# Kernel tuning notes

Hardware: AMD Instinct MI355X
Metric: run time of the kernel (lower is better)

The kernel has to match this reference:

```python
import jax, jax.numpy as jnp
import numpy as np

B, SE, SD, IN_DIM, D, DEPTH, H, DH, M, FF, NBINS = 8, 2048, 1024, 1280, 512, 4, 8, 64, 266, 2048, 128

def _ln(x, g, b):
    mu = x.mean(-1, keepdims=True)
    var = ((x - mu) ** 2).mean(-1, keepdims=True)
    return (x - mu) / jnp.sqrt(var + 1e-5) * g + b

def _gelu(x):
    return jax.nn.gelu(x, approximate=False)

def _sinusoidal(x, dim):
    # sinusoidal embedding of integer expression bins -> [.., dim]
    half = dim // 2
    freqs = jnp.exp(-jnp.log(10000.0) * jnp.arange(half, dtype=jnp.float32) / half)
    ang = x[..., None].astype(jnp.float32) * freqs
    return jnp.concatenate([jnp.sin(ang), jnp.cos(ang)], axis=-1)

def _split_heads(x):
    b, s, _ = x.shape
    return x.reshape(b, s, H, DH).transpose(0, 2, 1, 3)

def _merge_heads(x):
    b, h, s, d = x.shape
    return x.transpose(0, 2, 1, 3).reshape(b, s, h * d)

def _favor_attention(q, k, v, proj):
    # FAVOR+ softmax-kernel linear attention (non-causal), performer-style
    dn = DH ** -0.25
    ratio = M ** -0.5
    eps = 1e-4
    qd = jnp.einsum('bhsd,md->bhsm', q * dn, proj)
    kd = jnp.einsum('bhsd,md->bhsm', k * dn, proj)
    q_diag = 0.5 * (q ** 2).sum(-1, keepdims=True) * dn * dn
    k_diag = 0.5 * (k ** 2).sum(-1, keepdims=True) * dn * dn
    qp = ratio * (jnp.exp(qd - q_diag - jnp.max(qd, axis=-1, keepdims=True)) + eps)
    kp = ratio * (jnp.exp(kd - k_diag - jnp.max(kd)) + eps)
    k_sum = kp.sum(axis=2)                                   # [b,h,m]
    d_inv = 1.0 / jnp.einsum('bhsm,bhm->bhs', qp, k_sum)     # [b,h,s]
    kv = jnp.einsum('bhsm,bhsd->bhmd', kp, v)                # [b,h,m,d]
    return jnp.einsum('bhsm,bhmd->bhsd', qp, kv) * d_inv[..., None]

def _forward(var_input_encoder, var_input_decoder, var_W, var_b, enc_ln_g, enc_ln_b, dec_ln_g, dec_ln_b, p_ln1_g, p_ln1_b, p_Wq, p_Wk, p_Wv, p_Wo, p_bo, p_ln2_g, p_ln2_b, p_w1, p_b1, p_w2, p_b2, proj, ca_Wq, ca_Wk, ca_Wv, ca_Wo, ca_bo, cross_ln_g, cross_ln_b, ffd_w1, ffd_b1, ffd_w2, ffd_b2, out_ln_g, out_ln_b, head_W, head_b, expression_encoder):
    expr = _sinusoidal(expression_encoder, D)            # [B,SE,D]
    enc = var_input_encoder @ var_W + var_b              # [B,SE,D]
    dec = var_input_decoder @ var_W + var_b              # [B,SD,D]
    x = _ln(enc + expr, enc_ln_g, enc_ln_b)
    # Performer encoder: pre-LN self-attn (FAVOR+) + pre-LN FF, residuals
    for i in range(DEPTH):
        y = _ln(x, p_ln1_g[i], p_ln1_b[i])
        q = _split_heads(y @ p_Wq[i])
        k = _split_heads(y @ p_Wk[i])
        v = _split_heads(y @ p_Wv[i])
        x = x + (_merge_heads(_favor_attention(q, k, v, proj[i])) @ p_Wo[i] + p_bo[i])
        y = _ln(x, p_ln2_g[i], p_ln2_b[i])
        x = x + (_gelu(y @ p_w1[i] + p_b1[i]) @ p_w2[i] + p_b2[i])
    context = x
    # decoder: LN -> softmax cross-attention over encoder context
    dec = _ln(dec, dec_ln_g, dec_ln_b)
    q = _split_heads(dec @ ca_Wq)
    k = _split_heads(context @ ca_Wk)
    v = _split_heads(context @ ca_Wv)
    scores = jnp.einsum('bhqd,bhkd->bhqk', q, k) * (DH ** -0.5)
    o = _merge_heads(jnp.einsum('bhqk,bhkd->bhqd', jax.nn.softmax(scores, axis=-1), v)) @ ca_Wo + ca_bo
    out = _ln(o + dec, cross_ln_g, cross_ln_b)
    out = _gelu(out @ ffd_w1 + ffd_b1) @ ffd_w2 + ffd_b2   # note: no residual around FF (as in source)
    out = _ln(out, out_ln_g, out_ln_b)
    return out @ head_W + head_b                            # [B,SD,NBINS]

def setup_inputs() -> dict:
    key = jax.random.key(0)
    ks = iter(jax.random.split(key, 64))
    def w(shape, scale=0.02):
        return jax.random.normal(next(ks), shape, dtype=jnp.float32) * scale
    inp = {
        'var_input_encoder': jax.random.normal(next(ks), (B, SE, IN_DIM), dtype=jnp.float32),
        'var_input_decoder': jax.random.normal(next(ks), (B, SD, IN_DIM), dtype=jnp.float32),
        'expression_encoder': jax.random.randint(next(ks), (B, SE), 0, NBINS, dtype=jnp.int32),
        'var_W': w((IN_DIM, D)), 'var_b': jnp.zeros((D,), jnp.float32),
        'enc_ln_g': jnp.ones((D,), jnp.float32), 'enc_ln_b': jnp.zeros((D,), jnp.float32),
        'dec_ln_g': jnp.ones((D,), jnp.float32), 'dec_ln_b': jnp.zeros((D,), jnp.float32),
        'p_ln1_g': jnp.ones((DEPTH, D), jnp.float32), 'p_ln1_b': jnp.zeros((DEPTH, D), jnp.float32),
        'p_Wq': w((DEPTH, D, H * DH)), 'p_Wk': w((DEPTH, D, H * DH)), 'p_Wv': w((DEPTH, D, H * DH)),
        'p_Wo': w((DEPTH, H * DH, D)), 'p_bo': jnp.zeros((DEPTH, D), jnp.float32),
        'p_ln2_g': jnp.ones((DEPTH, D), jnp.float32), 'p_ln2_b': jnp.zeros((DEPTH, D), jnp.float32),
        'p_w1': w((DEPTH, D, FF)), 'p_b1': jnp.zeros((DEPTH, FF), jnp.float32),
        'p_w2': w((DEPTH, FF, D)), 'p_b2': jnp.zeros((DEPTH, D), jnp.float32),
        'proj': jax.random.normal(next(ks), (DEPTH, M, DH), dtype=jnp.float32),
        'ca_Wq': w((D, H * DH)), 'ca_Wk': w((D, H * DH)), 'ca_Wv': w((D, H * DH)),
        'ca_Wo': w((H * DH, D)), 'ca_bo': jnp.zeros((D,), jnp.float32),
        'cross_ln_g': jnp.ones((D,), jnp.float32), 'cross_ln_b': jnp.zeros((D,), jnp.float32),
        'ffd_w1': w((D, FF)), 'ffd_b1': jnp.zeros((FF,), jnp.float32),
        'ffd_w2': w((FF, D)), 'ffd_b2': jnp.zeros((D,), jnp.float32),
        'out_ln_g': jnp.ones((D,), jnp.float32), 'out_ln_b': jnp.zeros((D,), jnp.float32),
        'head_W': w((D, NBINS)), 'head_b': jnp.zeros((NBINS,), jnp.float32),
    }
    return inp

def reference(var_input_encoder, var_input_decoder, expression_encoder, var_W, var_b, enc_ln_g, enc_ln_b, dec_ln_g, dec_ln_b, p_ln1_g, p_ln1_b, p_Wq, p_Wk, p_Wv, p_Wo, p_bo, p_ln2_g, p_ln2_b, p_w1, p_b1, p_w2, p_b2, proj, ca_Wq, ca_Wk, ca_Wv, ca_Wo, ca_bo, cross_ln_g, cross_ln_b, ffd_w1, ffd_b1, ffd_w2, ffd_b2, out_ln_g, out_ln_b, head_W, head_b):
    return _forward(var_input_encoder, var_input_decoder, var_W, var_b, enc_ln_g, enc_ln_b, dec_ln_g, dec_ln_b, p_ln1_g, p_ln1_b, p_Wq, p_Wk, p_Wv, p_Wo, p_bo, p_ln2_g, p_ln2_b, p_w1, p_b1, p_w2, p_b2, proj, ca_Wq, ca_Wk, ca_Wv, ca_Wo, ca_bo, cross_ln_g, cross_ln_b, ffd_w1, ffd_b1, ffd_w2, ffd_b2, out_ln_g, out_ln_b, head_W, head_b, expression_encoder)
```

## Files before the change

### kernel.cpp

```cpp
#include <hip/hip_runtime.h>
#include <hip/hip_bf16.h>
#include <math.h>

constexpr int cB = 8, cSE = 2048, cSD = 1024, cIN = 1280, cD = 512,
              cDEPTH = 4, cH = 8, cDH = 64, cM = 266, cFF = 2048, cNB = 128;
constexpr int cMP = 288;

#define DEV __device__ __forceinline__

typedef __bf16 bf16;
typedef __attribute__((ext_vector_type(8))) __bf16 bf16x8;
typedef __attribute__((ext_vector_type(4))) __bf16 bf16x4;
typedef __attribute__((ext_vector_type(2))) __bf16 bf16x2;
typedef __attribute__((ext_vector_type(4))) float f32x4;

DEV float gelu_f(float x) { return 0.5f * x * (1.0f + erff(x * 0.70710678118654752440f)); }

DEV float wave_sum(float v) {
#pragma unroll
  for (int o = 32; o; o >>= 1) v += __shfl_xor(v, o);
  return v;
}
DEV float wave_max(float v) {
#pragma unroll
  for (int o = 32; o; o >>= 1) v = fmaxf(v, __shfl_xor(v, o));
  return v;
}

#define GL2LDS(gp, lp) __builtin_amdgcn_global_load_lds(                    \
    (const __attribute__((address_space(1))) void*)(gp),                    \
    (__attribute__((address_space(3))) void*)(lp), 16, 0, 0)

template <int OUT, int ACT, bool BIAS, bool RES>
__global__ __launch_bounds__(256) void gemm_mfma(
    const bf16* __restrict__ A, const bf16* __restrict__ Bt,
    void* __restrict__ Cv, bf16* __restrict__ Cv2,
    const float* __restrict__ bias, int M, int N, int K) {
  __shared__ bf16 As[2 * 128 * 32];
  __shared__ bf16 Bs[2 * 128 * 32];
  const int t = threadIdx.x, l = t & 63, w = t >> 6;
  const int g = l >> 4, c = l & 15;
  const int nwg = gridDim.x * gridDim.y;
  int id = blockIdx.y * gridDim.x + blockIdx.x;
  if ((nwg & 7) == 0) id = (id & 7) * (nwg >> 3) + (id >> 3);
  const int m0 = (id / gridDim.x) * 128, n0 = (id % gridDim.x) * 128;
  const int wr = (w >> 1) * 64, wc = (w & 1) * 64;
  const int srow = w * 32 + (l >> 2);
  const int scol = (l & 3) * 8;
  const bf16* gA = A + (size_t)(m0 + srow) * K + scol;
  const bf16* gB = Bt + (size_t)(n0 + srow) * K + scol;
  bf16* lA = As + w * 1024;
  bf16* lB = Bs + w * 1024;

  const f32x4 zero4 = {0.f, 0.f, 0.f, 0.f};
  f32x4 acc[4][4];
#pragma unroll
  for (int i = 0; i < 4; i++)
#pragma unroll
    for (int j = 0; j < 4; j++) acc[i][j] = zero4;

  for (int k0 = 0; k0 < K; k0 += 64) {
    GL2LDS(gA + k0, lA);
    GL2LDS(gA + (size_t)16 * K + k0, lA + 512);
    GL2LDS(gB + k0, lB);
    GL2LDS(gB + (size_t)16 * K + k0, lB + 512);
    GL2LDS(gA + k0 + 32, lA + 4096);
    GL2LDS(gA + (size_t)16 * K + k0 + 32, lA + 4096 + 512);
    GL2LDS(gB + k0 + 32, lB + 4096);
    GL2LDS(gB + (size_t)16 * K + k0 + 32, lB + 4096 + 512);
    __syncthreads();
#pragma unroll
    for (int hh = 0; hh < 2; hh++) {
      bf16x8 af[4], bfr[4];
#pragma unroll
      for (int i = 0; i < 4; i++)
        af[i] = *(const bf16x8*)(As + hh * 4096 + (wr + i * 16 + c) * 32 + g * 8);
#pragma unroll
      for (int j = 0; j < 4; j++)
        bfr[j] = *(const bf16x8*)(Bs + hh * 4096 + (wc + j * 16 + c) * 32 + g * 8);
#pragma unroll
      for (int i = 0; i < 4; i++)
#pragma unroll
        for (int j = 0; j < 4; j++)
          acc[i][j] = __builtin_amdgcn_mfma_f32_16x16x32_bf16(af[i], bfr[j], acc[i][j], 0, 0, 0);
    }
    __syncthreads();
  }
  float* Cf = (float*)Cv;
  bf16* Cb = (bf16*)Cv;
#pragma unroll
  for (int i = 0; i < 4; i++) {
    const int mb = m0 + wr + i * 16 + g * 4;
#pragma unroll
    for (int j = 0; j < 4; j++) {
      const int n = n0 + wc + j * 16 + c;
      const float bv = BIAS ? bias[n] : 0.f;
#pragma unroll
      for (int r = 0; r < 4; r++) {
        float v = acc[i][j][r] + bv;
        if (ACT == 1) v = gelu_f(v);
        if (ACT == 2) v *= 0.18033688011112042f;
        const size_t idx = (size_t)(mb + r) * N + n;
        if (OUT == 0) {
          float* cp = Cf + idx;
          if (RES) v += *cp;
          *cp = v;
        } else if (OUT == 3) {
          bf16* cp = Cb + idx;
          v += (float)*cp;
          *cp = (bf16)v;
        } else {
          Cb[idx] = (bf16)v;
        }
      }
    }
  }
}

__global__ __launch_bounds__(256) void mega_prep(
    const float* __restrict__ Wq, const float* __restrict__ Wk,
    const float* __restrict__ Wv, const float* __restrict__ Wo,
    const float* __restrict__ w1, const float* __restrict__ w2,
    const float* __restrict__ var_W, const float* __restrict__ proj,
    const float* __restrict__ in_enc, const float* __restrict__ in_dec,
    bf16* __restrict__ WL, bf16* __restrict__ WtVar,
    bf16* __restrict__ projB4, bf16* __restrict__ encB,
    bf16* __restrict__ decB) {
  const int z = blockIdx.y, bid = blockIdx.x, t = threadIdx.x;
  if (z >= 26) {
    const float* src = (z == 26) ? in_enc : in_dec;
    bf16* dst = (z == 26) ? encB : decB;
    const int n = (z == 26) ? 16384 * 1280 : 8192 * 1280;
    int i = (bid * 256 + t) * 4;
    const int stride = gridDim.x * 256 * 4;
    for (; i < n; i += stride) {
      float4 v = *(const float4*)(src + i);
      bf16x4 o;
      o[0] = (bf16)v.x; o[1] = (bf16)v.y; o[2] = (bf16)v.z; o[3] = (bf16)v.w;
      *(bf16x4*)(dst + i) = o;
    }
    return;
  }
  if (z == 25) {
    const int idx = bid * 256 + t;
    if (idx < 4 * cMP * cDH) {
      const int layer = idx / (cMP * cDH), r = idx % (cMP * cDH);
      const int m = r >> 6;
      projB4[idx] = (bf16)(m < cM ? proj[(size_t)layer * cM * cDH + r] * 0.35355339059327373f : 0.f);
    }
    return;
  }
  __shared__ float tile[32][33];
  const float* W;
  bf16* dst;
  int K, N;
  if (z == 24) {
    W = var_W; dst = WtVar; K = 1280; N = 512;
  } else {
    const int layer = z / 6, mat = z % 6;
    bf16* base = WL + (size_t)layer * 3145728;
    if (mat < 4) {
      W = (mat == 0 ? Wq : mat == 1 ? Wk : mat == 2 ? Wv : Wo) + (size_t)layer * 262144;
      dst = base + mat * 262144; K = 512; N = 512;
    } else if (mat == 4) {
      W = w1 + (size_t)layer * 1048576; dst = base + 1048576; K = 512; N = 2048;
    } else {
      W = w2 + (size_t)layer * 1048576; dst = base + 2097152; K = 2048; N = 512;
    }
  }
  const int nt = N >> 5;
  if (bid >= nt * (K >> 5)) return;
  const int n0 = (bid % nt) * 32, k0 = (bid / nt) * 32;
  const int tx = t & 31, ty = t >> 5;
#pragma unroll
  for (int i = ty; i < 32; i += 8) tile[i][tx] = W[(size_t)(k0 + i) * N + n0 + tx];
  __syncthreads();
#pragma unroll
  for (int i = ty; i < 32; i += 8)
    dst[(size_t)(n0 + i) * K + k0 + tx] = (bf16)tile[tx][i];
}

__global__ __launch_bounds__(256) void mega_prep_dec(
    const float* __restrict__ caWq, const float* __restrict__ caWk,
    const float* __restrict__ caWv, const float* __restrict__ caWo,
    const float* __restrict__ fw1, const float* __restrict__ fw2,
    const float* __restrict__ hW, bf16* __restrict__ WD) {
  const int z = blockIdx.y, bid = blockIdx.x, t = threadIdx.x;
  __shared__ float tile[32][33];
  const float* W;
  bf16* dst;
  int K, N;
  if (z < 4) {
    W = (z == 0 ? caWq : z == 1 ? caWk : z == 2 ? caWv : caWo);
    dst = WD + z * 262144; K = 512; N = 512;
  } else if (z == 4) {
    W = fw1; dst = WD + 1048576; K = 512; N = 2048;
  } else if (z == 5) {
    W = fw2; dst = WD + 2097152; K = 2048; N = 512;
  } else {
    W = hW; dst = WD + 3145728; K = 512; N = 128;
  }
  const int nt = N >> 5;
  if (bid >= nt * (K >> 5)) return;
  const int n0 = (bid % nt) * 32, k0 = (bid / nt) * 32;
  const int tx = t & 31, ty = t >> 5;
#pragma unroll
  for (int i = ty; i < 32; i += 8) tile[i][tx] = W[(size_t)(k0 + i) * N + n0 + tx];
  __syncthreads();
#pragma unroll
  for (int i = ty; i < 32; i += 8)
    dst[(size_t)(n0 + i) * K + k0 + tx] = (bf16)tile[tx][i];
}

__global__ __launch_bounds__(256) void favor_prep(
    const bf16* __restrict__ QKV, const bf16* __restrict__ projB,
    bf16* __restrict__ Vt, float* __restrict__ bmax) {
  const int z = blockIdx.y, b = z >> 3, h = z & 7;
  const int t = threadIdx.x;
  const int ld = 1536;
  if (blockIdx.x < 32) {
    __shared__ bf16 tile[64][65];
    const bf16* Vh = QKV + 1024;
    const int s0 = blockIdx.x * 64;
#pragma unroll
    for (int r = t >> 3; r < 64; r += 32) {
      bf16x8 v = *(const bf16x8*)(Vh + ((size_t)b * cSE + s0 + r) * ld + h * cDH + (t & 7) * 8);
#pragma unroll
      for (int e = 0; e < 8; e++) tile[(t & 7) * 8 + e][r] = v[e];
    }
    __syncthreads();
    bf16* vz = Vt + (size_t)z * 80 * cSE;
#pragma unroll
    for (int d = t >> 3; d < 64; d += 32) {
      bf16x8 o;
#pragma unroll
      for (int e = 0; e < 8; e++) o[e] = tile[d][(t & 7) * 8 + e];
      *(bf16x8*)(vz + (size_t)d * cSE + s0 + (t & 7) * 8) = o;
    }
    const int rr = t >> 4, seg = (t & 15) * 4;
    bf16x4 ov;
    const float val = (rr == 0) ? 1.f : 0.f;
    ov[0] = (bf16)val; ov[1] = (bf16)val; ov[2] = (bf16)val; ov[3] = (bf16)val;
    *(bf16x4*)(vz + (size_t)(64 + rr) * cSE + s0 + seg) = ov;
    return;
  }
  __shared__ float sm[4];
  const bf16* Kh = QKV + 512;
  const int xb = blockIdx.x - 32;
  const int s0 = xb * 128;
  const int l = t & 63, w = t >> 6, g = l >> 4, c = l & 15;
  const int wr = (w >> 1) * 64, wcol = (w & 1) * 144;
  const f32x4 zero4 = {0.f, 0.f, 0.f, 0.f};
  f32x4 acc[4][9];
#pragma unroll
  for (int i = 0; i < 4; i++)
#pragma unroll
    for (int j = 0; j < 9; j++) acc[i][j] = zero4;
  const size_t abase = ((size_t)b * cSE + s0) * ld + h * cDH;
#pragma unroll
  for (int k0 = 0; k0 < 64; k0 += 32) {
    bf16x8 af[4];
#pragma unroll
    for (int i = 0; i < 4; i++)
      af[i] = *(const bf16x8*)(Kh + abase + (size_t)(wr + i * 16 + c) * ld + k0 + g * 8);
#pragma unroll
    for (int j = 0; j < 9; j++) {
      bf16x8 bfr = *(const bf16x8*)(projB + (wcol + j * 16 + c) * 64 + k0 + g * 8);
#pragma unroll
      for (int i = 0; i < 4; i++)
        acc[i][j] = __builtin_amdgcn_mfma_f32_16x16x32_bf16(af[i], bfr, acc[i][j], 0, 0, 0);
    }
  }
  float m = -3e38f;
#pragma unroll
  for (int i = 0; i < 4; i++)
#pragma unroll
    for (int j = 0; j < 9; j++) {
      const int mc = wcol + j * 16 + c;
      if (mc < cM) {
#pragma unroll
        for (int r = 0; r < 4; r++) m = fmaxf(m, acc[i][j][r]);
      }
    }
  m = wave_max(m);
  if (l == 0) sm[w] = m;
  __syncthreads();
  if (t == 0)
    bmax[z * 16 + xb] = fmaxf(fmaxf(sm[0], sm[1]), fmaxf(sm[2], sm[3]));
}

__global__ __launch_bounds__(256, 1) void favor_kkv(
    const bf16* __restrict__ Kh, int ld, const bf16* __restrict__ projB,
    const bf16* __restrict__ Vt, const float* __restrict__ bmax,
    bf16* __restrict__ part) {
  __shared__ bf16 kp[288 * 72];
  __shared__ float sm[4];
  const int z = blockIdx.y, b = z >> 3, h = z & 7;
  const int chunk = blockIdx.x;
  const int t = threadIdx.x, l = t & 63, w = t >> 6, g = l >> 4, c = l & 15;
  float gm;
  {
    float m = -1e30f;
    for (int i = t; i < 1024; i += 256) m = fmaxf(m, bmax[i]);
    m = wave_max(m);
    if (l == 0) sm[w] = m;
    __syncthreads();
    gm = fmaxf(fmaxf(sm[0], sm[1]), fmaxf(sm[2], sm[3]));
  }
  const int pr = (w >> 1) * 32;
  const int wcol = (w & 1) * 144;
  const int wm = (w & 1) * 144, wd = (w >> 1) * 32;
  const bool dden = (wd == 32);
  const float ratio = 0.061313927f;
  const f32x4 zero4 = {0.f, 0.f, 0.f, 0.f};
  f32x4 kacc[9][2], kaccx[9];
#pragma unroll
  for (int j = 0; j < 9; j++) {
    kacc[j][0] = zero4; kacc[j][1] = zero4; kaccx[j] = zero4;
  }
  const size_t kbase = (size_t)b * cSE * ld + h * cDH;
  const size_t vtz = (size_t)z * 80 * cSE;

  bf16x8 afp[4];
  auto LOADK = [&](int sg) {
#pragma unroll
    for (int k0i = 0; k0i < 2; k0i++)
#pragma unroll
      for (int i = 0; i < 2; i++)
        afp[k0i * 2 + i] = *(const bf16x8*)(Kh + kbase +
            (size_t)(sg + pr + i * 16 + c) * ld + k0i * 32 + g * 8);
  };
  LOADK(chunk * 256);

  for (int st = 0; st < 256; st += 64) {
    const int sg = chunk * 256 + st;
    bf16x8 af[4];
#pragma unroll
    for (int q = 0; q < 4; q++) af[q] = afp[q];
    if (st + 64 < 256) LOADK(sg + 64);
    f32x4 pacc[2][9];
#pragma unroll
    for (int i = 0; i < 2; i++)
#pragma unroll
      for (int j = 0; j < 9; j++) pacc[i][j] = zero4;
    float sq[2] = {0.f, 0.f};
#pragma unroll
    for (int k0i = 0; k0i < 2; k0i++) {
#pragma unroll
      for (int i = 0; i < 2; i++) {
#pragma unroll
        for (int e = 0; e < 8; e++) {
          const float v = (float)af[k0i * 2 + i][e];
          sq[i] += v * v;
        }
      }
#pragma unroll
      for (int j = 0; j < 9; j++) {
        bf16x8 bfr = *(const bf16x8*)(projB + (wcol + j * 16 + c) * 64 + k0i * 32 + g * 8);
        pacc[0][j] = __builtin_amdgcn_mfma_f32_16x16x32_bf16(af[k0i * 2 + 0], bfr, pacc[0][j], 0, 0, 0);
        pacc[1][j] = __builtin_amdgcn_mfma_f32_16x16x32_bf16(af[k0i * 2 + 1], bfr, pacc[1][j], 0, 0, 0);
      }
    }
#pragma unroll
    for (int i = 0; i < 2; i++) {
      sq[i] += __shfl_xor(sq[i], 16);
      sq[i] += __shfl_xor(sq[i], 32);
    }
    float rowsub[2][4];
#pragma unroll
    for (int i = 0; i < 2; i++)
#pragma unroll
      for (int r = 0; r < 4; r++)
        rowsub[i][r] = gm + 0.0625f * __shfl(sq[i], g * 4 + r);
    __syncthreads();
#pragma unroll
    for (int i = 0; i < 2; i++)
#pragma unroll
      for (int j = 0; j < 9; j++) {
        const int mc = wcol + j * 16 + c;
        bf16x4 o;
#pragma unroll
        for (int r = 0; r < 4; r++) {
          const float v = (mc < cM)
              ? ratio * (__expf(pacc[i][j][r] - rowsub[i][r]) + 1e-4f) : 0.f;
          o[r] = (bf16)v;
        }
        *(bf16x4*)(kp + (size_t)mc * 72 + pr + i * 16 + g * 4) = o;
      }
    __syncthreads();
#pragma unroll
    for (int k0 = 0; k0 < 64; k0 += 32) {
      bf16x8 bv0 = *(const bf16x8*)(Vt + vtz + (size_t)(wd + c) * cSE + sg + k0 + g * 8);
      bf16x8 bv1 = *(const bf16x8*)(Vt + vtz + (size_t)(wd + 16 + c) * cSE + sg + k0 + g * 8);
      bf16x8 bvx;
      if (dden)
        bvx = *(const bf16x8*)(Vt + vtz + (size_t)(64 + c) * cSE + sg + k0 + g * 8);
#pragma unroll
      for (int j = 0; j < 9; j++) {
        bf16x8 am = *(const bf16x8*)(kp + (size_t)(wm + j * 16 + c) * 72 + k0 + g * 8);
        kacc[j][0] = __builtin_amdgcn_mfma_f32_16x16x32_bf16(am, bv0, kacc[j][0], 0, 0, 0);
        kacc[j][1] = __builtin_amdgcn_mfma_f32_16x16x32_bf16(am, bv1, kacc[j][1], 0, 0, 0);
        if (dden)
          kaccx[j] = __builtin_amdgcn_mfma_f32_16x16x32_bf16(am, bvx, kaccx[j], 0, 0, 0);
      }
    }
  }
  bf16* po = part + ((size_t)z * 8 + chunk) * (cMP * 80);
#pragma unroll
  for (int j = 0; j < 9; j++)
#pragma unroll
    for (int i = 0; i < 2; i++)
#pragma unroll
      for (int r = 0; r < 4; r++)
        po[(size_t)(wm + j * 16 + g * 4 + r) * 80 + wd + i * 16 + c] = (bf16)kacc[j][i][r];
  if (dden) {
#pragma unroll
    for (int j = 0; j < 9; j++)
#pragma unroll
      for (int r = 0; r < 4; r++)
        po[(size_t)(wm + j * 16 + g * 4 + r) * 80 + 64 + c] = (bf16)kaccx[j][r];
  }
}

__global__ __launch_bounds__(256) void kv_reduce(
    const bf16* __restrict__ part, bf16* __restrict__ kvT) {
  const int z = blockIdx.y, q = blockIdx.x;
  const bf16* p = part + (size_t)z * 8 * (cMP * 80);
  bf16* o = kvT + (size_t)z * 80 * cMP;
  const int lo = q * 5760, hi = lo + 5760;
  for (int idx = lo + threadIdx.x; idx < hi; idx += 256) {
    const int m = idx / 80, d = idx - m * 80;
    float s = 0.f;
#pragma unroll
    for (int cc = 0; cc < 8; cc++) s += (float)p[idx + (size_t)cc * (cMP * 80)];
    o[(size_t)d * cMP + m] = (bf16)s;
  }
}

__global__ __launch_bounds__(256, 1) void favor_qout(
    const bf16* __restrict__ Qh, int ld, const bf16* __restrict__ projB,
    const bf16* __restrict__ kvT, bf16* __restrict__ Y) {
  __shared__ bf16 Plds[128 * 296];
  __shared__ float rmaxs[4][64];
  __shared__ float denl[128];
  const int z = blockIdx.y, b = z >> 3, h = z & 7;
  const int s0 = blockIdx.x * 128;
  const int t = threadIdx.x, l = t & 63, w = t >> 6, g = l >> 4, c = l & 15;
  const int wr = (w >> 1) * 64, wcol = (w & 1) * 144;
  const f32x4 zero4 = {0.f, 0.f, 0.f, 0.f};
  f32x4 acc[4][9];
#pragma unroll
  for (int i = 0; i < 4; i++)
#pragma unroll
    for (int j = 0; j < 9; j++) acc[i][j] = zero4;
  float sq[4] = {0.f, 0.f, 0.f, 0.f};
  const size_t abase = ((size_t)b * cSE + s0) * ld + h * cDH;
#pragma unroll
  for (int k0 = 0; k0 < 64; k0 += 32) {
    bf16x8 af[4];
#pragma unroll
    for (int i = 0; i < 4; i++) {
      af[i] = *(const bf16x8*)(Qh + abase + (size_t)(wr + i * 16 + c) * ld + k0 + g * 8);
#pragma unroll
      for (int e = 0; e < 8; e++) {
        const float v = (float)af[i][e];
        sq[i] += v * v;
      }
    }
#pragma unroll
    for (int j = 0; j < 9; j++) {
      bf16x8 bfr = *(const bf16x8*)(projB + (wcol + j * 16 + c) * 64 + k0 + g * 8);
#pragma unroll
      for (int i = 0; i < 4; i++)
        acc[i][j] = __builtin_amdgcn_mfma_f32_16x16x32_bf16(af[i], bfr, acc[i][j], 0, 0, 0);
    }
  }
#pragma unroll
  for (int i = 0; i < 4; i++) {
    sq[i] += __shfl_xor(sq[i], 16);
    sq[i] += __shfl_xor(sq[i], 32);
  }
  const float ratio = 0.061313927f;
  float rowsub[4][4];
#pragma unroll
  for (int i = 0; i < 4; i++)
#pragma unroll
    for (int r = 0; r < 4; r++) {
      float m = -3e38f;
#pragma unroll
      for (int j = 0; j < 9; j++) {
        const int mc = wcol + j * 16 + c;
        m = (mc < cM) ? fmaxf(m, acc[i][j][r]) : m;
      }
      m = fmaxf(m, __shfl_xor(m, 1));
      m = fmaxf(m, __shfl_xor(m, 2));
      m = fmaxf(m, __shfl_xor(m, 4));
      m = fmaxf(m, __shfl_xor(m, 8));
      rowsub[i][r] = m;
    }
  if (c == 0) {
#pragma unroll
    for (int i = 0; i < 4; i++)
#pragma unroll
      for (int r = 0; r < 4; r++) rmaxs[w][i * 16 + g * 4 + r] = rowsub[i][r];
  }
  __syncthreads();
#pragma unroll
  for (int i = 0; i < 4; i++)
#pragma unroll
    for (int r = 0; r < 4; r++) {
      const int row = i * 16 + g * 4 + r;
      rowsub[i][r] = fmaxf(rowsub[i][r], rmaxs[w ^ 1][row]) +
                     0.0625f * __shfl(sq[i], g * 4 + r);
    }
#pragma unroll
  for (int i = 0; i < 4; i++)
#pragma unroll
    for (int j = 0; j < 9; j++) {
      const int mc = wcol + j * 16 + c;
#pragma unroll
      for (int r = 0; r < 4; r++) {
        const float v = (mc < cM)
            ? ratio * (__expf(acc[i][j][r] - rowsub[i][r]) + 1e-4f) : 0.f;
        Plds[(wr + i * 16 + g * 4 + r) * 296 + mc] = (bf16)v;
      }
    }
  __syncthreads();

  const int wd = (w & 1) * 32;
  const bool dden = (wd == 32);
  f32x4 acc2[4][2], accx[4];
#pragma unroll
  for (int i = 0; i < 4; i++) {
    acc2[i][0] = zero4; acc2[i][1] = zero4; accx[i] = zero4;
  }
  const size_t kz = (size_t)z * 80 * cMP;
#pragma unroll 3
  for (int k0 = 0; k0 < cMP; k0 += 32) {
    bf16x8 bv[2], bvx;
#pragma unroll
    for (int j = 0; j < 2; j++)
      bv[j] = *(const bf16x8*)(kvT + kz + (size_t)(wd + j * 16 + c) * cMP + k0 + g * 8);
    if (dden)
      bvx = *(const bf16x8*)(kvT + kz + (size_t)(64 + c) * cMP + k0 + g * 8);
#pragma unroll
    for (int i = 0; i < 4; i++) {
      bf16x8 av = *(const bf16x8*)(Plds + (wr + i * 16 + c) * 296 + k0 + g * 8);
      acc2[i][0] = __builtin_amdgcn_mfma_f32_16x16x32_bf16(av, bv[0], acc2[i][0], 0, 0, 0);
      acc2[i][1] = __builtin_amdgcn_mfma_f32_16x16x32_bf16(av, bv[1], acc2[i][1], 0, 0, 0);
      if (dden)
        accx[i] = __builtin_amdgcn_mfma_f32_16x16x32_bf16(av, bvx, accx[i], 0, 0, 0);
    }
  }
  if (dden && c == 0) {
#pragma unroll
    for (int i = 0; i < 4; i++)
#pragma unroll
      for (int r = 0; r < 4; r++)
        denl[wr + i * 16 + g * 4 + r] = accx[i][r];
  }
  __syncthreads();
#pragma unroll
  for (int i = 0; i < 4; i++)
#pragma unroll
    for (int r = 0; r < 4; r++) {
      const int row = wr + i * 16 + g * 4 + r;
      const float inv = 1.0f / denl[row];
#pragma unroll
      for (int j = 0; j < 2; j++)
        Y[((size_t)b * cSE + s0 + row) * cD + h * cDH + wd + j * 16 + c] =
            (bf16)(acc2[i][j][r] * inv);
    }
}

template <bool ADD>
__global__ __launch_bounds__(256) void ln_rows_b(
    const bf16* __restrict__ in, const bf16* __restrict__ add,
    const float* __restrict__ g, const float* __restrict__ be,
    bf16* __restrict__ out) {
  const int wid = blockIdx.x * 4 + (threadIdx.x >> 6);
  const int lane = threadIdx.x & 63;
  bf16x8 iv = *(const bf16x8*)(in + (size_t)wid * cD + lane * 8);
  float x[8];
#pragma unroll
  for (int i = 0; i < 8; i++) x[i] = (float)iv[i];
  if (ADD) {
    bf16x8 av = *(const bf16x8*)(add + (size_t)wid * cD + lane * 8);
#pragma unroll
    for (int i = 0; i < 8; i++) x[i] += (float)av[i];
  }
  float s = 0;
#pragma unroll
  for (int i = 0; i < 8; i++) s += x[i];
  s = wave_sum(s);
  const float mu = s * (1.0f / cD);
  float vs = 0;
#pragma unroll
  for (int i = 0; i < 8; i++) { const float d = x[i] - mu; vs += d * d; }
  vs = wave_sum(vs);
  const float rstd = 1.0f / sqrtf(vs * (1.0f / cD) + 1e-5f);
  bf16x8 ov;
#pragma unroll
  for (int i = 0; i < 8; i++) {
    const int d = lane * 8 + i;
    ov[i] = (bf16)((x[i] - mu) * rstd * g[d] + be[d]);
  }
  *(bf16x8*)(out + (size_t)wid * cD + lane * 8) = ov;
}

__global__ __launch_bounds__(256) void embed_ln_b(
    bf16* __restrict__ X, const int* __restrict__ ids,
    const float* __restrict__ g, const float* __restrict__ be) {
  const int wid = blockIdx.x * 4 + (threadIdx.x >> 6);
  const int lane = threadIdx.x & 63;
  const float idv = (float)ids[wid];
  bf16* xp = X + (size_t)wid * cD + lane * 8;
  bf16x8 iv = *(const bf16x8*)xp;
  float x[8];
#pragma unroll
  for (int i = 0; i < 8; i++) x[i] = (float)iv[i];
  const float kf = -0.03597789207803197f;
#pragma unroll
  for (int i = 0; i < 8; i++) {
    const int d = lane * 8 + i;
    float e;
    if (d < 256) e = sinf(idv * expf(kf * (float)d));
    else         e = cosf(idv * expf(kf * (float)(d - 256)));
    x[i] += e;
  }
  float s = 0;
#pragma unroll
  for (int i = 0; i < 8; i++) s += x[i];
  s = wave_sum(s);
  const float mu = s * (1.0f / cD);
  float vs = 0;
#pragma unroll
  for (int i = 0; i < 8; i++) { const float d = x[i] - mu; vs += d * d; }
  vs = wave_sum(vs);
  const float rstd = 1.0f / sqrtf(vs * (1.0f / cD) + 1e-5f);
  bf16x8 ov;
#pragma unroll
  for (int i = 0; i < 8; i++) {
    const int d = lane * 8 + i;
    ov[i] = (bf16)((x[i] - mu) * rstd * g[d] + be[d]);
  }
  *(bf16x8*)xp = ov;
}

__global__ __launch_bounds__(256) void flash_mfma(
    const bf16* __restrict__ Q, const bf16* __restrict__ Kc,
    const bf16* __restrict__ Vc, bf16* __restrict__ O, int ldkv) {
  __shared__ __align__(16) bf16 KP[4 * 16 * 136];
  __shared__ __align__(16) bf16 Vs[80 * 136];
  const int id = blockIdx.x;
  const int b = (id & 63) >> 3, h = id & 7, qb = id >> 6;
  const int t = threadIdx.x, l = t & 63, w = t >> 6, g = l >> 4, c = l & 15;
  const int q0 = qb * 64 + w * 16;
  bf16x8 aq[2];
  {
    const bf16* qp = Q + ((size_t)b * cSD + q0 + c) * cD + h * cDH + g * 8;
    aq[0] = *(const bf16x8*)qp;
    aq[1] = *(const bf16x8*)(qp + 32);
  }
  for (int idx = t; idx < 16 * 136; idx += 256) {
    const int rr = idx / 136, cc = idx - rr * 136;
    Vs[(64 + rr) * 136 + cc] = (bf16)(rr == 0 ? 1.f : 0.f);
  }
  const f32x4 zero4 = {0.f, 0.f, 0.f, 0.f};
  f32x4 o5[5];
#pragma unroll
  for (int j = 0; j < 5; j++) o5[j] = zero4;
  float mrow[4];
#pragma unroll
  for (int r = 0; r < 4; r++) mrow[r] = -1e30f;

  const int kr = t >> 1, kof = (t & 1) * 32;
  const int sidx = t & 31, dseg = t >> 5;
  const size_t kvbase = (size_t)b * cSE * ldkv + h * cDH;
  char* KsC = (char*)KP;
  bf16* Pw = KP + w * 16 * 136;
  const float T2 = 11.541560327111708f;

  bf16x8 pk[4], pv[4];
  auto LOADR = [&](int kt) {
    const bf16* kp = Kc + kvbase + (size_t)(kt + kr) * ldkv + kof;
#pragma unroll
    for (int i = 0; i < 4; i++) pk[i] = *(const bf16x8*)(kp + i * 8);
    const bf16* vp = Vc + kvbase + (size_t)(kt + 4 * sidx) * ldkv + dseg * 8;
#pragma unroll
    for (int i = 0; i < 4; i++) pv[i] = *(const bf16x8*)(vp + (size_t)i * ldkv);
  };
  auto WRITEL = [&]() {
    const int sw = (kr & 7) << 4;
#pragma unroll
    for (int i = 0; i < 4; i++)
      *(bf16x8*)(KsC + kr * 128 + (((kof + i * 8) * 2) ^ sw)) = pk[i];
#pragma unroll
    for (int e = 0; e < 8; e++) {
      bf16x4 q4;
      q4[0] = pv[0][e]; q4[1] = pv[1][e]; q4[2] = pv[2][e]; q4[3] = pv[3][e];
      *(bf16x4*)(Vs + (dseg * 8 + e) * 136 + 4 * sidx) = q4;
    }
  };
  LOADR(0);
  WRITEL();

  for (int kt = 0; kt < cSE; kt += 128) {
    const bool more = (kt + 128 < cSE);
    if (more) LOADR(kt + 128);
    __syncthreads();
    f32x4 s4[8];
    __builtin_amdgcn_s_setprio(1);
#pragma unroll
    for (int t2 = 0; t2 < 8; t2++) {
      const int kr2 = t2 * 16 + c;
      const int sw2 = (kr2 & 7) << 4;
      bf16x8 bk0 = *(const bf16x8*)(KsC + kr2 * 128 + ((g * 16) ^ sw2));
      bf16x8 bk1 = *(const bf16x8*)(KsC + kr2 * 128 + ((64 + g * 16) ^ sw2));
      f32x4 z = zero4;
      z = __builtin_amdgcn_mfma_f32_16x16x32_bf16(aq[0], bk0, z, 0, 0, 0);
      z = __builtin_amdgcn_mfma_f32_16x16x32_bf16(aq[1], bk1, z, 0, 0, 0);
      s4[t2] = z;
    }
    __builtin_amdgcn_s_setprio(0);
    __syncthreads();
#pragma unroll
    for (int r = 0; r < 4; r++) {
      float xv[8];
#pragma unroll
      for (int t2 = 0; t2 < 8; t2++) xv[t2] = s4[t2][r];
      float tm = xv[0];
#pragma unroll
      for (int t2 = 1; t2 < 8; t2++) tm = fmaxf(tm, xv[t2]);
      tm = fmaxf(tm, __shfl_xor(tm, 1));
      tm = fmaxf(tm, __shfl_xor(tm, 2));
      tm = fmaxf(tm, __shfl_xor(tm, 4));
      tm = fmaxf(tm, __shfl_xor(tm, 8));
      if (tm > mrow[r] + T2) {
        const float corr = exp2f(mrow[r] - tm);
        mrow[r] = tm;
#pragma unroll
        for (int j = 0; j < 5; j++) o5[j][r] *= corr;
      }
      const float m = mrow[r];
      const int qr = g * 4 + r;
#pragma unroll
      for (int t2 = 0; t2 < 8; t2++)
        Pw[qr * 136 + t2 * 16 + c] = (bf16)exp2f(xv[t2] - m);
    }
    bf16x8 pa[4];
#pragma unroll
    for (int ks = 0; ks < 4; ks++)
      pa[ks] = *(const bf16x8*)(Pw + c * 136 + ks * 32 + g * 8);
    __builtin_amdgcn_s_setprio(1);
#pragma unroll
    for (int j = 0; j < 5; j++) {
#pragma unroll
      for (int ks = 0; ks < 4; ks++) {
        bf16x8 bv = *(const bf16x8*)(Vs + (j * 16 + c) * 136 + ks * 32 + g * 8);
        o5[j] = __builtin_amdgcn_mfma_f32_16x16x32_bf16(pa[ks], bv, o5[j], 0, 0, 0);
      }
    }
    __builtin_amdgcn_s_setprio(0);
    __syncthreads();
    if (more) WRITEL();
  }
#pragma unroll
  for (int r = 0; r < 4; r++) {
    const float den = __shfl(o5[4][r], l & 48);
    const float inv = 1.0f / den;
    const size_t row = (size_t)b * cSD + q0 + g * 4 + r;
#pragma unroll
    for (int j = 0; j < 4; j++)
      O[row * cD + h * cDH + j * 16 + c] = (bf16)(o5[j][r] * inv);
  }
}

extern "C" void kernel_launch(void* const* d_in, const int* in_sizes, int n_in,
                              void* d_out, int out_size, void* d_ws, size_t ws_size,
                              hipStream_t stream) {
  const float* in_enc = (const float*)d_in[0];
  const float* in_dec = (const float*)d_in[1];
  const int* expr = (const int*)d_in[2];
  const float* var_W = (const float*)d_in[3];
  const float* var_b = (const float*)d_in[4];
  const float* enc_g = (const float*)d_in[5];
  const float* enc_b = (const float*)d_in[6];
  const float* dec_g = (const float*)d_in[7];
  const float* dec_b = (const float*)d_in[8];
  const float* ln1_g = (const float*)d_in[9];
  const float* ln1_b = (const float*)d_in[10];
  const float* Wq = (const float*)d_in[11];
  const float* Wk = (const float*)d_in[12];
  const float* Wv = (const float*)d_in[13];
  const float* Wo = (const float*)d_in[14];
  const float* bo = (const float*)d_in[15];
  const float* ln2_g = (const float*)d_in[16];
  const float* ln2_b = (const float*)d_in[17];
  const float* w1 = (const float*)d_in[18];
  const float* b1 = (const float*)d_in[19];
  const float* w2 = (const float*)d_in[20];
  const float* b2 = (const float*)d_in[21];
  const float* proj = (const float*)d_in[22];
  const float* caWq = (const float*)d_in[23];
  const float* caWk = (const float*)d_in[24];
  const float* caWv = (const float*)d_in[25];
  const float* caWo = (const float*)d_in[26];
  const float* cabo = (const float*)d_in[27];
  const float* crg = (const float*)d_in[28];
  const float* crb = (const float*)d_in[29];
  const float* fw1 = (const float*)d_in[30];
  const float* fb1 = (const float*)d_in[31];
  const float* fw2 = (const float*)d_in[32];
  const float* fb2 = (const float*)d_in[33];
  const float* og = (const float*)d_in[34];
  const float* ob = (const float*)d_in[35];
  const float* hW = (const float*)d_in[36];
  const float* hb = (const float*)d_in[37];

  float* base  = (float*)d_ws;
  bf16*  Xr    = (bf16*)base;
  bf16*  Dt1   = Xr + 8388608;
  bf16*  Dt2   = Dt1 + 4194304;
  bf16*  QKV   = (bf16*)(base + 12582912);
  bf16*  Vt    = QKV + 25165824;
  bf16*  Pb    = Vt + 10485760;
  float* part  = (float*)(Pb + 50331648);
  bf16*  kvT   = (bf16*)(part + 11796480);
  float* bmax  = (float*)(kvT + 1474560);
  bf16*  Yb    = (bf16*)(bmax + 1040);
  bf16*  DCb   = Yb + 8388608;
  bf16*  Wt    = DCb + 4194304;
  bf16*  projB4 = Wt + 1048576;
  const size_t need_bytes = (size_t)75458576 * 4;
  if (ws_size < need_bytes) return;

  bf16* partB = (bf16*)part;
  bf16* encB = Pb;
  bf16* decB = (bf16*)part;
  bf16* Pmid = Pb;
  bf16* WL   = Pb + 33554432;
  bf16* Qc   = Pb + 8388608;
  bf16* KVc  = Pb + 12582912;
  bf16* Fb   = Pb + 29360128;
  bf16* Pm2  = Pb + 33554432;
  bf16* WD   = (bf16*)part;

  const dim3 blk(256);

  mega_prep<<<dim3(2048, 28), blk, 0, stream>>>(Wq, Wk, Wv, Wo, w1, w2, var_W, proj,
                                                in_enc, in_dec, WL, Wt, projB4,
                                                encB, decB);
  gemm_mfma<1, 0, true, false><<<dim3(4, 128), blk, 0, stream>>>(encB, Wt, Xr, nullptr, var_b, 16384, 512, 1280);
  gemm_mfma<1, 0, true, false><<<dim3(4, 64), blk, 0, stream>>>(decB, Wt, Dt1, nullptr, var_b, 8192, 512, 1280);
  embed_ln_b<<<4096, blk, 0, stream>>>(Xr, expr, enc_g, enc_b);
  ln_rows_b<false><<<2048, blk, 0, stream>>>(Dt1, nullptr, dec_g, dec_b, DCb);

  for (int i = 0; i < cDEPTH; i++) {
    bf16* Wl = WL + (size_t)i * 3145728;
    bf16* projB = projB4 + (size_t)i * (cMP * cDH);
    ln_rows_b<false><<<4096, blk, 0, stream>>>(Xr, nullptr, ln1_g + i * cD, ln1_b + i * cD, Yb);
    gemm_mfma<1, 0, false, false><<<dim3(12, 128), blk, 0, stream>>>(Yb, Wl, QKV, nullptr, nullptr, 16384, 1536, 512);
    favor_prep<<<dim3(48, 64), blk, 0, stream>>>(QKV, projB, Vt, bmax);
    favor_kkv<<<dim3(8, 64), blk, 0, stream>>>(QKV + 512, 1536, projB, Vt, bmax, partB);
    kv_reduce<<<dim3(4, 64), blk, 0, stream>>>(partB, kvT);
    favor_qout<<<dim3(16, 64), blk, 0, stream>>>(QKV, 1536, projB, kvT, Yb);
    gemm_mfma<3, 0, true, false><<<dim3(4, 128), blk, 0, stream>>>(Yb, Wl + 786432, Xr, nullptr, bo + i * cD, 16384, 512, 512);
    ln_rows_b<false><<<4096, blk, 0, stream>>>(Xr, nullptr, ln2_g + i * cD, ln2_b + i * cD, Yb);
    gemm_mfma<1, 1, true, false><<<dim3(16, 128), blk, 0, stream>>>(Yb, Wl + 1048576, Pmid, nullptr, b1 + i * cFF, 16384, 2048, 512);
    gemm_mfma<3, 0, true, false><<<dim3(4, 128), blk, 0, stream>>>(Pmid, Wl + 2097152, Xr, nullptr, b2 + i * cD, 16384, 512, 2048);
  }

  mega_prep_dec<<<dim3(1024, 7), blk, 0, stream>>>(caWq, caWk, caWv, caWo, fw1, fw2, hW, WD);
  gemm_mfma<1, 2, false, false><<<dim3(4, 64), blk, 0, stream>>>(DCb, WD, Qc, nullptr, nullptr, 8192, 512, 512);
  gemm_mfma<1, 0, false, false><<<dim3(8, 128), blk, 0, stream>>>(Xr, WD + 262144, KVc, nullptr, nullptr, 16384, 1024, 512);
  flash_mfma<<<dim3(1024), blk, 0, stream>>>(Qc, KVc, KVc + 512, Fb, 1024);
  gemm_mfma<1, 0, true, false><<<dim3(4, 64), blk, 0, stream>>>(Fb, WD + 786432, Dt1, nullptr, cabo, 8192, 512, 512);
  ln_rows_b<true><<<2048, blk, 0, stream>>>(Dt1, DCb, crg, crb, Yb);
  gemm_mfma<1, 1, true, false><<<dim3(16, 64), blk, 0, stream>>>(Yb, WD + 1048576, Pm2, nullptr, fb1, 8192, 2048, 512);
  gemm_mfma<1, 0, true, false><<<dim3(4, 64), blk, 0, stream>>>(Pm2, WD + 2097152, Dt2, nullptr, fb2, 8192, 512, 2048);
  ln_rows_b<false><<<2048, blk, 0, stream>>>(Dt2, nullptr, og, ob, Yb);
  gemm_mfma<0, 0, true, false><<<dim3(1, 64), blk, 0, stream>>>(Yb, WD + 3145728, (float*)d_out, nullptr, hb, 8192, 128, 512);
}
```

Baseline: 1.822 ms.

## Merge decoder weight prep into mega_prep, batch enc/dec input GEMM, use exp2

```diff
diff --git a/kernel.cpp b/kernel.cpp
--- a/kernel.cpp
+++ b/kernel.cpp
@@ -123,11 +123,15 @@
     const float* __restrict__ w1, const float* __restrict__ w2,
     const float* __restrict__ var_W, const float* __restrict__ proj,
     const float* __restrict__ in_enc, const float* __restrict__ in_dec,
+    const float* __restrict__ caWq, const float* __restrict__ caWk,
+    const float* __restrict__ caWv, const float* __restrict__ caWo,
+    const float* __restrict__ fw1, const float* __restrict__ fw2,
+    const float* __restrict__ hW,
     bf16* __restrict__ WL, bf16* __restrict__ WtVar,
     bf16* __restrict__ projB4, bf16* __restrict__ encB,
-    bf16* __restrict__ decB) {
+    bf16* __restrict__ decB, bf16* __restrict__ WD) {
   const int z = blockIdx.y, bid = blockIdx.x, t = threadIdx.x;
-  if (z >= 26) {
+  if (z == 26 || z == 27) {
     const float* src = (z == 26) ? in_enc : in_dec;
     bf16* dst = (z == 26) ? encB : decB;
     const int n = (z == 26) ? 16384 * 1280 : 8192 * 1280;
@@ -146,7 +150,7 @@
     if (idx < 4 * cMP * cDH) {
       const int layer = idx / (cMP * cDH), r = idx % (cMP * cDH);
       const int m = r >> 6;
-      projB4[idx] = (bf16)(m < cM ? proj[(size_t)layer * cM * cDH + r] * 0.35355339059327373f : 0.f);
+      projB4[idx] = (bf16)(m < cM ? proj[(size_t)layer * cM * cDH + r] * 0.51006972f : 0.f);
     }
     return;
   }
@@ -156,7 +160,7 @@
   int K, N;
   if (z == 24) {
     W = var_W; dst = WtVar; K = 1280; N = 512;
-  } else {
+  } else if (z < 24) {
     const int layer = z / 6, mat = z % 6;
     bf16* base = WL + (size_t)layer * 3145728;
     if (mat < 4) {
@@ -167,38 +171,18 @@
     } else {
       W = w2 + (size_t)layer * 1048576; dst = base + 2097152; K = 2048; N = 512;
     }
-  }
-  const int nt = N >> 5;
-  if (bid >= nt * (K >> 5)) return;
-  const int n0 = (bid % nt) * 32, k0 = (bid / nt) * 32;
-  const int tx = t & 31, ty = t >> 5;
-#pragma unroll
-  for (int i = ty; i < 32; i += 8) tile[i][tx] = W[(size_t)(k0 + i) * N + n0 + tx];
-  __syncthreads();
-#pragma unroll
-  for (int i = ty; i < 32; i += 8)
-    dst[(size_t)(n0 + i) * K + k0 + tx] = (bf16)tile[tx][i];
-}
-
-__global__ __launch_bounds__(256) void mega_prep_dec(
-    const float* __restrict__ caWq, const float* __restrict__ caWk,
-    const float* __restrict__ caWv, const float* __restrict__ caWo,
-    const float* __restrict__ fw1, const float* __restrict__ fw2,
-    const float* __restrict__ hW, bf16* __restrict__ WD) {
-  const int z = blockIdx.y, bid = blockIdx.x, t = threadIdx.x;
-  __shared__ float tile[32][33];
-  const float* W;
-  bf16* dst;
-  int K, N;
-  if (z < 4) {
-    W = (z == 0 ? caWq : z == 1 ? caWk : z == 2 ? caWv : caWo);
-    dst = WD + z * 262144; K = 512; N = 512;
-  } else if (z == 4) {
-    W = fw1; dst = WD + 1048576; K = 512; N = 2048;
-  } else if (z == 5) {
-    W = fw2; dst = WD + 2097152; K = 2048; N = 512;
   } else {
-    W = hW; dst = WD + 3145728; K = 512; N = 128;
+    const int d = z - 28;
+    if (d < 4) {
+      W = (d == 0 ? caWq : d == 1 ? caWk : d == 2 ? caWv : caWo);
+      dst = WD + d * 262144; K = 512; N = 512;
+    } else if (d == 4) {
+      W = fw1; dst = WD + 1048576; K = 512; N = 2048;
+    } else if (d == 5) {
+      W = fw2; dst = WD + 2097152; K = 2048; N = 512;
+    } else {
+      W = hW; dst = WD + 3145728; K = 512; N = 128;
+    }
   }
   const int nt = N >> 5;
   if (bid >= nt * (K >> 5)) return;
@@ -312,6 +296,7 @@
   const int wm = (w & 1) * 144, wd = (w >> 1) * 32;
   const bool dden = (wd == 32);
   const float ratio = 0.061313927f;
+  const float DIAG2 = 0.09016844f;
   const f32x4 zero4 = {0.f, 0.f, 0.f, 0.f};
   f32x4 kacc[9][2], kaccx[9];
 #pragma unroll
@@ -371,7 +356,7 @@
     for (int i = 0; i < 2; i++)
 #pragma unroll
       for (int r = 0; r < 4; r++)
-        rowsub[i][r] = gm + 0.0625f * __shfl(sq[i], g * 4 + r);
+        rowsub[i][r] = gm + DIAG2 * __shfl(sq[i], g * 4 + r);
     __syncthreads();
 #pragma unroll
     for (int i = 0; i < 2; i++)
@@ -382,7 +367,7 @@
 #pragma unroll
         for (int r = 0; r < 4; r++) {
           const float v = (mc < cM)
-              ? ratio * (__expf(pacc[i][j][r] - rowsub[i][r]) + 1e-4f) : 0.f;
+              ? ratio * (exp2f(pacc[i][j][r] - rowsub[i][r]) + 1e-4f) : 0.f;
           o[r] = (bf16)v;
         }
         *(bf16x4*)(kp + (size_t)mc * 72 + pr + i * 16 + g * 4) = o;
@@ -481,6 +466,7 @@
     sq[i] += __shfl_xor(sq[i], 32);
   }
   const float ratio = 0.061313927f;
+  const float DIAG2 = 0.09016844f;
   float rowsub[4][4];
 #pragma unroll
   for (int i = 0; i < 4; i++)
@@ -511,7 +497,7 @@
     for (int r = 0; r < 4; r++) {
       const int row = i * 16 + g * 4 + r;
       rowsub[i][r] = fmaxf(rowsub[i][r], rmaxs[w ^ 1][row]) +
-                     0.0625f * __shfl(sq[i], g * 4 + r);
+                     DIAG2 * __shfl(sq[i], g * 4 + r);
     }
 #pragma unroll
   for (int i = 0; i < 4; i++)
@@ -521,7 +507,7 @@
 #pragma unroll
       for (int r = 0; r < 4; r++) {
         const float v = (mc < cM)
-            ? ratio * (__expf(acc[i][j][r] - rowsub[i][r]) + 1e-4f) : 0.f;
+            ? ratio * (exp2f(acc[i][j][r] - rowsub[i][r]) + 1e-4f) : 0.f;
         Plds[(wr + i * 16 + g * 4 + r) * 296 + mc] = (bf16)v;
       }
     }
@@ -837,22 +823,22 @@
 
   bf16* partB = (bf16*)part;
   bf16* encB = Pb;
-  bf16* decB = (bf16*)part;
+  bf16* decB = Pb + 20971520;
   bf16* Pmid = Pb;
   bf16* WL   = Pb + 33554432;
+  bf16* WD   = Pb + 46137344;
   bf16* Qc   = Pb + 8388608;
   bf16* KVc  = Pb + 12582912;
   bf16* Fb   = Pb + 29360128;
-  bf16* Pm2  = Pb + 33554432;
-  bf16* WD   = (bf16*)part;
+  bf16* Pm2  = Pb + 8388608;
 
   const dim3 blk(256);
 
-  mega_prep<<<dim3(2048, 28), blk, 0, stream>>>(Wq, Wk, Wv, Wo, w1, w2, var_W, proj,
-                                                in_enc, in_dec, WL, Wt, projB4,
-                                                encB, decB);
-  gemm_mfma<1, 0, true, false><<<dim3(4, 128), blk, 0, stream>>>(encB, Wt, Xr, nullptr, var_b, 16384, 512, 1280);
-  gemm_mfma<1, 0, true, false><<<dim3(4, 64), blk, 0, stream>>>(decB, Wt, Dt1, nullptr, var_b, 8192, 512, 1280);
+  mega_prep<<<dim3(2048, 35), blk, 0, stream>>>(
+      Wq, Wk, Wv, Wo, w1, w2, var_W, proj, in_enc, in_dec,
+      caWq, caWk, caWv, caWo, fw1, fw2, hW,
+      WL, Wt, projB4, encB, decB, WD);
+  gemm_mfma<1, 0, true, false><<<dim3(4, 192), blk, 0, stream>>>(encB, Wt, Xr, nullptr, var_b, 24576, 512, 1280);
   embed_ln_b<<<4096, blk, 0, stream>>>(Xr, expr, enc_g, enc_b);
   ln_rows_b<false><<<2048, blk, 0, stream>>>(Dt1, nullptr, dec_g, dec_b, DCb);
 
@@ -871,7 +857,6 @@
     gemm_mfma<3, 0, true, false><<<dim3(4, 128), blk, 0, stream>>>(Pmid, Wl + 2097152, Xr, nullptr, b2 + i * cD, 16384, 512, 2048);
   }
 
-  mega_prep_dec<<<dim3(1024, 7), blk, 0, stream>>>(caWq, caWk, caWv, caWo, fw1, fw2, hW, WD);
   gemm_mfma<1, 2, false, false><<<dim3(4, 64), blk, 0, stream>>>(DCb, WD, Qc, nullptr, nullptr, 8192, 512, 512);
   gemm_mfma<1, 0, false, false><<<dim3(8, 128), blk, 0, stream>>>(Xr, WD + 262144, KVc, nullptr, nullptr, 16384, 1024, 512);
   flash_mfma<<<dim3(1024), blk, 0, stream>>>(Qc, KVc, KVc + 512, Fb, 1024);
```

After: 1.841 ms. Within noise of the previous version (+1.0%).
